# Performance work log

Measured on AMD Instinct MI355X. Metric: run time of the kernel, lower is better.

## Reference

```python
import jax, jax.numpy as jnp
import numpy as np
import math

INF = 10000000000.0
D_KEY = 64


def setup_inputs() -> dict:
    key = jax.random.key(0)
    kq, kk, kv = jax.random.split(key, 3)
    B, S, D = 4, 4096, D_KEY
    return {
        "query": jax.random.normal(kq, (B, S, D), dtype=jnp.float32),
        "key": jax.random.normal(kk, (B, S, D), dtype=jnp.float32),
        "value": jax.random.normal(kv, (B, S, D), dtype=jnp.float32),
    }


def reference(query, key, value):
    # dot_products: [B, Sq, Sk]
    scale = math.sqrt(D_KEY)
    scores = jnp.einsum("bqd,bkd->bqk", query, key)
    S = key.shape[1]
    # causal: subtract INF on strict upper triangle (triu(1)), before scaling
    tri = jnp.triu(jnp.full((S, S), INF, dtype=scores.dtype), k=1)
    scores = scores - tri[None, :, :]
    logits = scores / scale
    probs = jax.nn.softmax(logits, axis=-1)  # softmax over key dim
    # dropout p=0.0 -> identity
    return jnp.einsum("bqk,bkd->bqd", probs, value)
```

## Files before the change

kernel.cpp:

```cpp
#include <hip/hip_runtime.h>
#include <hip/hip_bf16.h>
#include <math.h>

#define B_  4
#define S_  4096
#define D_  64
#define NQT 64
#define NST 32
#define LDP 68
#define QSC 0.18033688f
#define M0  20.0f

typedef __attribute__((ext_vector_type(8))) short bf16x8;
typedef __attribute__((ext_vector_type(4))) float f32x4;
typedef __attribute__((ext_vector_type(4))) short short4v;

static __device__ inline short f2bf(float f) {
    union { float f; unsigned u; } v; v.f = f;
    unsigned u = v.u;
    unsigned r = u + 0x7fff + ((u >> 16) & 1);
    return (short)(r >> 16);
}
static __device__ inline float bf2f(short s) {
    union { unsigned u; float f; } v; v.u = ((unsigned)(unsigned short)s) << 16;
    return v.f;
}
static __device__ inline unsigned cvt_pk_bf16(float lo, float hi) {
    unsigned r;
    asm("v_cvt_pk_bf16_f32 %0, %1, %2" : "=v"(r) : "v"(lo), "v"(hi));
    return r;
}

__global__ __launch_bounds__(256) void fa_prep(const float* __restrict__ K,
                                               const float* __restrict__ V,
                                               short* __restrict__ Kbf,
                                               short* __restrict__ Vtbf)
{
    const int b   = blockIdx.x >> 6;
    const int st  = blockIdx.x & 63;
    const int tid = threadIdx.x;
    __shared__ short Vs[64 * 72];

    const size_t tbase = ((size_t)b * S_ + (size_t)st * 64) * D_;
    #pragma unroll
    for (int rr = 0; rr < 4; ++rr) {
        int i = tid + rr * 256;
        size_t e = tbase + (size_t)i * 4;
        f32x4 k = *(const f32x4*)(K + e);
        union { short4v s; unsigned u[2]; } ks;
        ks.u[0] = cvt_pk_bf16(k[0], k[1]);
        ks.u[1] = cvt_pk_bf16(k[2], k[3]);
        *(short4v*)(Kbf + e) = ks.s;
        f32x4 v = *(const f32x4*)(V + e);
        int key = i >> 4, d4 = (i & 15) * 4;
        Vs[(d4 + 0) * 72 + key] = f2bf(v[0]);
        Vs[(d4 + 1) * 72 + key] = f2bf(v[1]);
        Vs[(d4 + 2) * 72 + key] = f2bf(v[2]);
        Vs[(d4 + 3) * 72 + key] = f2bf(v[3]);
    }
    __syncthreads();
    #pragma unroll
    for (int cc = 0; cc < 2; ++cc) {
        int c = tid + cc * 256;
        int d = c >> 3, sg = c & 7;
        bf16x8 row = *(const bf16x8*)&Vs[d * 72 + sg * 8];
        *(bf16x8*)(Vtbf + ((size_t)(b * D_ + d)) * S_ + (size_t)st * 64 + sg * 8) = row;
    }
}

__global__ __launch_bounds__(512) void fa_part(const float* __restrict__ Qf,
                                               const short* __restrict__ Kbf,
                                               const short* __restrict__ Vtbf,
                                               short* __restrict__ Opart,
                                               float* __restrict__ Lpart,
                                               int CH, int T)
{
    const int bid = blockIdx.x;
    const int b   = bid / T;
    int r = bid - b * T;
    int qt2 = NST - 1;
    while (true) {
        int n = (2 * qt2 + 2 + CH - 1) / CH;
        if (r < n) break;
        r -= n; --qt2;
    }
    const int kt0 = r * CH;
    const int nkt = 2 * qt2 + 2;
    const int kt1 = (kt0 + CH < nkt) ? kt0 + CH : nkt;

    const int tid  = threadIdx.x;
    const int wave = tid >> 6;
    const int lane = tid & 63;
    const int lm   = lane & 15;
    const int lk   = lane >> 4;

    __shared__ __align__(16) short Ks[2][64 * 64];
    __shared__ __align__(16) short Vt[2][64 * 64];
    __shared__ __align__(16) short Ps[128 * LDP];

    bf16x8 qA[2];
    {
        const float* qp = Qf + ((size_t)(b * S_ + qt2 * 128 + wave * 16 + lm)) * D_;
        #pragma unroll
        for (int h = 0; h < 2; ++h) {
            f32x4 a0 = *(const f32x4*)(qp + h * 32 + lk * 8);
            f32x4 a1 = *(const f32x4*)(qp + h * 32 + lk * 8 + 4);
            union { bf16x8 v; unsigned u[4]; } qa;
            qa.u[0] = cvt_pk_bf16(a0[0] * QSC, a0[1] * QSC);
            qa.u[1] = cvt_pk_bf16(a0[2] * QSC, a0[3] * QSC);
            qa.u[2] = cvt_pk_bf16(a1[0] * QSC, a1[1] * QSC);
            qa.u[3] = cvt_pk_bf16(a1[2] * QSC, a1[3] * QSC);
            qA[h] = qa.v;
        }
    }

    bf16x8 onesF;
    #pragma unroll
    for (int j = 0; j < 8; ++j) onesF[j] = (short)0x3F80;

    const int srow = tid >> 3;
    const int sseg = (tid & 7) ^ (srow & 7);
    const char* kgp = (const char*)(Kbf + (size_t)b * S_ * D_)
                    + (size_t)(kt0 * 64 + srow) * 128 + sseg * 16;
    const char* vgp = (const char*)(Vtbf + ((size_t)(b * D_ + srow)) * S_)
                    + (size_t)kt0 * 128 + sseg * 16;

    bf16x8 kreg = *(const bf16x8*)kgp;
    bf16x8 vreg = *(const bf16x8*)vgp;
    kgp += 8192; vgp += 128;
    *(bf16x8*)&Ks[0][tid * 8] = kreg;
    *(bf16x8*)&Vt[0][tid * 8] = vreg;
    __syncthreads();
    if (kt0 + 1 < kt1) {
        kreg = *(const bf16x8*)kgp;
        vreg = *(const bf16x8*)vgp;
        kgp += 8192; vgp += 128;
    }

    f32x4 l4 = (f32x4){0.f, 0.f, 0.f, 0.f};
    f32x4 o_acc[4];
    #pragma unroll
    for (int dt = 0; dt < 4; ++dt) o_acc[dt] = (f32x4){0.f, 0.f, 0.f, 0.f};

    const int wrow = wave * 16 + lk * 4;
    int cur = 0;

    for (int kt = kt0; kt < kt1; ++kt) {
        f32x4 s4[4];
        __builtin_amdgcn_s_setprio(1);
        #pragma unroll
        for (int ct = 0; ct < 4; ++ct) {
            f32x4 acc = (f32x4){-M0, -M0, -M0, -M0};
            #pragma unroll
            for (int h = 0; h < 2; ++h) {
                int seg = (h * 4 + lk) ^ (lm & 7);
                bf16x8 bF = *(const bf16x8*)&Ks[cur][(ct * 16 + lm) * 64 + seg * 8];
                acc = __builtin_amdgcn_mfma_f32_16x16x32_bf16(qA[h], bF, acc, 0, 0, 0);
            }
            s4[ct] = acc;
        }
        __builtin_amdgcn_s_setprio(0);

        if (kt >= 2 * qt2) {
            const int koff = kt * 64 - qt2 * 128;
            #pragma unroll
            for (int ct = 0; ct < 4; ++ct) {
                #pragma unroll
                for (int rr = 0; rr < 4; ++rr) {
                    if (koff + ct * 16 + lm > wrow + rr) s4[ct][rr] = -INFINITY;
                }
            }
        }

        #pragma unroll
        for (int ct = 0; ct < 4; ++ct) {
            #pragma unroll
            for (int rr = 0; rr < 4; ++rr) s4[ct][rr] = exp2f(s4[ct][rr]);
        }
        #pragma unroll
        for (int ct = 0; ct < 4; ++ct) {
            unsigned p01 = cvt_pk_bf16(s4[ct][0], s4[ct][1]);
            unsigned p23 = cvt_pk_bf16(s4[ct][2], s4[ct][3]);
            Ps[(wrow + 0) * LDP + ct * 16 + lm] = (short)(p01 & 0xffff);
            Ps[(wrow + 1) * LDP + ct * 16 + lm] = (short)(p01 >> 16);
            Ps[(wrow + 2) * LDP + ct * 16 + lm] = (short)(p23 & 0xffff);
            Ps[(wrow + 3) * LDP + ct * 16 + lm] = (short)(p23 >> 16);
        }
        bf16x8 aF[2];
        #pragma unroll
        for (int kh = 0; kh < 2; ++kh)
            aF[kh] = *(const bf16x8*)&Ps[(wave * 16 + lm) * LDP + kh * 32 + lk * 8];
        __builtin_amdgcn_s_setprio(1);
        #pragma unroll
        for (int kh = 0; kh < 2; ++kh)
            l4 = __builtin_amdgcn_mfma_f32_16x16x32_bf16(aF[kh], onesF, l4, 0, 0, 0);
        #pragma unroll
        for (int dt = 0; dt < 4; ++dt) {
            #pragma unroll
            for (int kh = 0; kh < 2; ++kh) {
                int seg = (kh * 4 + lk) ^ (lm & 7);
                bf16x8 bF = *(const bf16x8*)&Vt[cur][(dt * 16 + lm) * 64 + seg * 8];
                o_acc[dt] = __builtin_amdgcn_mfma_f32_16x16x32_bf16(aF[kh], bF, o_acc[dt], 0, 0, 0);
            }
        }
        __builtin_amdgcn_s_setprio(0);

        if (kt + 1 < kt1) {
            *(bf16x8*)&Ks[cur ^ 1][tid * 8] = kreg;
            *(bf16x8*)&Vt[cur ^ 1][tid * 8] = vreg;
            __syncthreads();
            if (kt + 2 < kt1) {
                kreg = *(const bf16x8*)kgp;
                vreg = *(const bf16x8*)vgp;
                kgp += 8192; vgp += 128;
            }
            cur ^= 1;
        }
    }

    short* Op = Opart + (size_t)bid * (128 * D_);
    if (lm == 0) {
        #pragma unroll
        for (int rr = 0; rr < 4; ++rr)
            Lpart[(size_t)bid * 128 + wrow + rr] = l4[rr];
    }
    #pragma unroll
    for (int dt = 0; dt < 4; ++dt) {
        unsigned o01 = cvt_pk_bf16(o_acc[dt][0], o_acc[dt][1]);
        unsigned o23 = cvt_pk_bf16(o_acc[dt][2], o_acc[dt][3]);
        Op[(wrow + 0) * D_ + dt * 16 + lm] = (short)(o01 & 0xffff);
        Op[(wrow + 1) * D_ + dt * 16 + lm] = (short)(o01 >> 16);
        Op[(wrow + 2) * D_ + dt * 16 + lm] = (short)(o23 & 0xffff);
        Op[(wrow + 3) * D_ + dt * 16 + lm] = (short)(o23 >> 16);
    }
}

__global__ __launch_bounds__(256) void fa_combine(const short* __restrict__ Opart,
                                                  const float* __restrict__ Lpart,
                                                  float* __restrict__ O,
                                                  int CH, int T)
{
    const int idx = blockIdx.x * 256 + threadIdx.x;
    const int b   = idx / (S_ * 16);
    const int rem = idx - b * (S_ * 16);
    const int q   = rem >> 4;
    const int d4  = (rem & 15) << 2;
    const int qt2 = q >> 7;
    const int rit = q & 127;

    int F = 0;
    for (int y = qt2 + 1; y < NST; ++y) F += (2 * y + 2 + CH - 1) / CH;
    const int base = b * T + F;
    const int nch  = (2 * qt2 + 2 + CH - 1) / CH;

    float L = 0.f;
    f32x4 acc = (f32x4){0.f, 0.f, 0.f, 0.f};
    for (int c = 0; c < nch; ++c) {
        L += Lpart[(size_t)(base + c) * 128 + rit];
        short4v o = *(const short4v*)(Opart + (size_t)(base + c) * (128 * D_) + rit * D_ + d4);
        acc[0] += bf2f(o[0]); acc[1] += bf2f(o[1]);
        acc[2] += bf2f(o[2]); acc[3] += bf2f(o[3]);
    }
    float inv = 1.f / L;
    f32x4 outv;
    outv[0] = acc[0] * inv; outv[1] = acc[1] * inv;
    outv[2] = acc[2] * inv; outv[3] = acc[3] * inv;
    *(f32x4*)(O + (size_t)idx * 4) = outv;
}

__global__ __launch_bounds__(256) void fa_fwd(const float* __restrict__ Q,
                                              const float* __restrict__ K,
                                              const float* __restrict__ V,
                                              float* __restrict__ O)
{
    const int qt   = (gridDim.x - 1) - blockIdx.x;
    const int b    = blockIdx.y;
    const int tid  = threadIdx.x;
    const int wave = tid >> 6;
    const int lane = tid & 63;
    const int lm   = lane & 15;
    const int lk   = lane >> 4;

    __shared__ short Ks[64 * 72];
    __shared__ short Vt[64 * 72];
    __shared__ short Ps[64 * 72];

    const float* Qb = Q + ((size_t)b * S_ + (size_t)qt * 64) * D_;
    const float* Kb = K + (size_t)b * S_ * D_;
    const float* Vb = V + (size_t)b * S_ * D_;

    bf16x8 qA[2];
    {
        const float* qp = Qb + (wave * 16 + lm) * D_;
        #pragma unroll
        for (int h = 0; h < 2; ++h) {
            const float* p = qp + h * 32 + lk * 8;
            #pragma unroll
            for (int j = 0; j < 8; ++j) qA[h][j] = f2bf(p[j] * 0.125f);
        }
    }
    float m_i[4], l_i[4];
    f32x4 o_acc[4];
    #pragma unroll
    for (int rr = 0; rr < 4; ++rr) { m_i[rr] = -INFINITY; l_i[rr] = 0.f; }
    #pragma unroll
    for (int dt = 0; dt < 4; ++dt) o_acc[dt] = (f32x4){0.f, 0.f, 0.f, 0.f};

    const int n_kt = qt + 1;
    for (int kt = 0; kt < n_kt; ++kt) {
        __syncthreads();
        #pragma unroll
        for (int rr = 0; rr < 4; ++rr) {
            int i   = tid + rr * 256;
            int row = i >> 4;
            int c4  = (i & 15) * 4;
            const size_t gbase = ((size_t)(kt * 64 + row)) * D_ + c4;
            f32x4 kv = *(const f32x4*)(Kb + gbase);
            short4v ks;
            ks[0] = f2bf(kv[0]); ks[1] = f2bf(kv[1]);
            ks[2] = f2bf(kv[2]); ks[3] = f2bf(kv[3]);
            *(short4v*)&Ks[row * 72 + c4] = ks;
            f32x4 vv = *(const f32x4*)(Vb + gbase);
            Vt[(c4 + 0) * 72 + row] = f2bf(vv[0]);
            Vt[(c4 + 1) * 72 + row] = f2bf(vv[1]);
            Vt[(c4 + 2) * 72 + row] = f2bf(vv[2]);
            Vt[(c4 + 3) * 72 + row] = f2bf(vv[3]);
        }
        __syncthreads();
        f32x4 s4[4];
        #pragma unroll
        for (int ct = 0; ct < 4; ++ct) {
            f32x4 acc = (f32x4){0.f, 0.f, 0.f, 0.f};
            #pragma unroll
            for (int h = 0; h < 2; ++h) {
                bf16x8 bF = *(const bf16x8*)&Ks[(ct * 16 + lm) * 72 + h * 32 + lk * 8];
                acc = __builtin_amdgcn_mfma_f32_16x16x32_bf16(qA[h], bF, acc, 0, 0, 0);
            }
            s4[ct] = acc;
        }
        if (kt == qt) {
            #pragma unroll
            for (int ct = 0; ct < 4; ++ct) {
                #pragma unroll
                for (int rr = 0; rr < 4; ++rr) {
                    int qrow = wave * 16 + lk * 4 + rr;
                    int kcol = ct * 16 + lm;
                    if (kcol > qrow) s4[ct][rr] = -INFINITY;
                }
            }
        }
        float alpha[4];
        #pragma unroll
        for (int rr = 0; rr < 4; ++rr) {
            float mx = fmaxf(fmaxf(s4[0][rr], s4[1][rr]), fmaxf(s4[2][rr], s4[3][rr]));
            mx = fmaxf(mx, __shfl_xor(mx, 1));
            mx = fmaxf(mx, __shfl_xor(mx, 2));
            mx = fmaxf(mx, __shfl_xor(mx, 4));
            mx = fmaxf(mx, __shfl_xor(mx, 8));
            float mn = fmaxf(m_i[rr], mx);
            alpha[rr] = __expf(m_i[rr] - mn);
            m_i[rr] = mn;
        }
        float rsum[4] = {0.f, 0.f, 0.f, 0.f};
        #pragma unroll
        for (int ct = 0; ct < 4; ++ct) {
            #pragma unroll
            for (int rr = 0; rr < 4; ++rr) {
                float p = __expf(s4[ct][rr] - m_i[rr]);
                s4[ct][rr] = p;
                rsum[rr] += p;
            }
        }
        #pragma unroll
        for (int rr = 0; rr < 4; ++rr) {
            float rs = rsum[rr];
            rs += __shfl_xor(rs, 1);
            rs += __shfl_xor(rs, 2);
            rs += __shfl_xor(rs, 4);
            rs += __shfl_xor(rs, 8);
            l_i[rr] = l_i[rr] * alpha[rr] + rs;
        }
        #pragma unroll
        for (int ct = 0; ct < 4; ++ct) {
            #pragma unroll
            for (int rr = 0; rr < 4; ++rr) {
                Ps[(wave * 16 + lk * 4 + rr) * 72 + ct * 16 + lm] = f2bf(s4[ct][rr]);
            }
        }
        #pragma unroll
        for (int dt = 0; dt < 4; ++dt) {
            #pragma unroll
            for (int rr = 0; rr < 4; ++rr) o_acc[dt][rr] *= alpha[rr];
        }
        #pragma unroll
        for (int dt = 0; dt < 4; ++dt) {
            #pragma unroll
            for (int kh = 0; kh < 2; ++kh) {
                bf16x8 aF = *(const bf16x8*)&Ps[(wave * 16 + lm) * 72 + kh * 32 + lk * 8];
                bf16x8 bF = *(const bf16x8*)&Vt[(dt * 16 + lm) * 72 + kh * 32 + lk * 8];
                o_acc[dt] = __builtin_amdgcn_mfma_f32_16x16x32_bf16(aF, bF, o_acc[dt], 0, 0, 0);
            }
        }
    }
    float* Ob = O + ((size_t)b * S_ + (size_t)qt * 64) * D_;
    #pragma unroll
    for (int rr = 0; rr < 4; ++rr) {
        float inv = 1.f / l_i[rr];
        int row = wave * 16 + lk * 4 + rr;
        #pragma unroll
        for (int dt = 0; dt < 4; ++dt) {
            Ob[row * D_ + dt * 16 + lm] = o_acc[dt][rr] * inv;
        }
    }
}

extern "C" void kernel_launch(void* const* d_in, const int* in_sizes, int n_in,
                              void* d_out, int out_size, void* d_ws, size_t ws_size,
                              hipStream_t stream) {
    const float* Q = (const float*)d_in[0];
    const float* K = (const float*)d_in[1];
    const float* V = (const float*)d_in[2];
    float* O = (float*)d_out;

    const size_t convShorts = (size_t)B_ * S_ * D_;
    int CH = 0, T = 0;
    const int chs[5] = {6, 8, 16, 32, 64};
    for (int k = 0; k < 5; ++k) {
        int c = chs[k];
        int t = 0;
        for (int q2 = 0; q2 < NST; ++q2) t += (2 * q2 + 2 + c - 1) / c;
        size_t need = 2 * convShorts * 2
                    + (size_t)B_ * t * (128 * D_) * 2
                    + (size_t)B_ * t * 128 * 4;
        if (need <= ws_size) { CH = c; T = t; break; }
    }
    if (CH == 0) {
        dim3 grid(NQT, B_);
        fa_fwd<<<grid, 256, 0, stream>>>(Q, K, V, O);
        return;
    }
    short* Kbf   = (short*)d_ws;
    short* Vtbf  = Kbf + convShorts;
    short* Opart = Vtbf + convShorts;
    float* Lpart = (float*)(Opart + (size_t)B_ * T * (128 * D_));

    fa_prep<<<dim3(B_ * NQT), 256, 0, stream>>>(K, V, Kbf, Vtbf);
    fa_part<<<dim3(B_ * T), 512, 0, stream>>>(Q, Kbf, Vtbf, Opart, Lpart, CH, T);
    fa_combine<<<dim3((B_ * S_ * 16) / 256), 256, 0, stream>>>(Opart, Lpart, O, CH, T);
}
```

Before: 99.15 us.

## Compute transposed S tiles so P stays in registers, dropping the LDS round-trip

The QK^T MFMA now swaps its operands so each lane holds a row of the score tile laid out like the A operand of the PV MFMA. The probabilities are packed into bf16 fragments directly in registers instead of being written to and read back from shared memory. The V transpose in the prep kernel permutes key order within each tile to match this fragment layout, and the causal mask indexing is adjusted accordingly. It also removes the Ps LDS buffer and adds an occupancy hint to launch bounds, which may raise register pressure or cause spills.

```diff
diff --git a/kernel.cpp b/kernel.cpp
--- a/kernel.cpp
+++ b/kernel.cpp
@@ -7,7 +7,6 @@
 #define D_  64
 #define NQT 64
 #define NST 32
-#define LDP 68
 #define QSC 0.18033688f
 #define M0  20.0f
 
@@ -53,10 +52,11 @@
         *(short4v*)(Kbf + e) = ks.s;
         f32x4 v = *(const f32x4*)(V + e);
         int key = i >> 4, d4 = (i & 15) * 4;
-        Vs[(d4 + 0) * 72 + key] = f2bf(v[0]);
-        Vs[(d4 + 1) * 72 + key] = f2bf(v[1]);
-        Vs[(d4 + 2) * 72 + key] = f2bf(v[2]);
-        Vs[(d4 + 3) * 72 + key] = f2bf(v[3]);
+        int slot = (key & 32) + (((key & 15) >> 2) << 3) + (((key >> 4) & 1) << 2) + (key & 3);
+        Vs[(d4 + 0) * 72 + slot] = f2bf(v[0]);
+        Vs[(d4 + 1) * 72 + slot] = f2bf(v[1]);
+        Vs[(d4 + 2) * 72 + slot] = f2bf(v[2]);
+        Vs[(d4 + 3) * 72 + slot] = f2bf(v[3]);
     }
     __syncthreads();
     #pragma unroll
@@ -68,7 +68,7 @@
     }
 }
 
-__global__ __launch_bounds__(512) void fa_part(const float* __restrict__ Qf,
+__global__ __launch_bounds__(512, 6) void fa_part(const float* __restrict__ Qf,
                                                const short* __restrict__ Kbf,
                                                const short* __restrict__ Vtbf,
                                                short* __restrict__ Opart,
@@ -96,7 +96,6 @@
 
     __shared__ __align__(16) short Ks[2][64 * 64];
     __shared__ __align__(16) short Vt[2][64 * 64];
-    __shared__ __align__(16) short Ps[128 * LDP];
 
     bf16x8 qA[2];
     {
@@ -143,6 +142,7 @@
     for (int dt = 0; dt < 4; ++dt) o_acc[dt] = (f32x4){0.f, 0.f, 0.f, 0.f};
 
     const int wrow = wave * 16 + lk * 4;
+    const int qrow = wave * 16 + lm;
     int cur = 0;
 
     for (int kt = kt0; kt < kt1; ++kt) {
@@ -154,20 +154,20 @@
             #pragma unroll
             for (int h = 0; h < 2; ++h) {
                 int seg = (h * 4 + lk) ^ (lm & 7);
-                bf16x8 bF = *(const bf16x8*)&Ks[cur][(ct * 16 + lm) * 64 + seg * 8];
-                acc = __builtin_amdgcn_mfma_f32_16x16x32_bf16(qA[h], bF, acc, 0, 0, 0);
+                bf16x8 kF = *(const bf16x8*)&Ks[cur][(ct * 16 + lm) * 64 + seg * 8];
+                acc = __builtin_amdgcn_mfma_f32_16x16x32_bf16(kF, qA[h], acc, 0, 0, 0);
             }
             s4[ct] = acc;
         }
         __builtin_amdgcn_s_setprio(0);
 
         if (kt >= 2 * qt2) {
-            const int koff = kt * 64 - qt2 * 128;
+            const int koff = kt * 64 - qt2 * 128 + lk * 4;
             #pragma unroll
             for (int ct = 0; ct < 4; ++ct) {
                 #pragma unroll
                 for (int rr = 0; rr < 4; ++rr) {
-                    if (koff + ct * 16 + lm > wrow + rr) s4[ct][rr] = -INFINITY;
+                    if (koff + ct * 16 + rr > qrow) s4[ct][rr] = -INFINITY;
                 }
             }
         }
@@ -177,19 +177,16 @@
             #pragma unroll
             for (int rr = 0; rr < 4; ++rr) s4[ct][rr] = exp2f(s4[ct][rr]);
         }
-        #pragma unroll
-        for (int ct = 0; ct < 4; ++ct) {
-            unsigned p01 = cvt_pk_bf16(s4[ct][0], s4[ct][1]);
-            unsigned p23 = cvt_pk_bf16(s4[ct][2], s4[ct][3]);
-            Ps[(wrow + 0) * LDP + ct * 16 + lm] = (short)(p01 & 0xffff);
-            Ps[(wrow + 1) * LDP + ct * 16 + lm] = (short)(p01 >> 16);
-            Ps[(wrow + 2) * LDP + ct * 16 + lm] = (short)(p23 & 0xffff);
-            Ps[(wrow + 3) * LDP + ct * 16 + lm] = (short)(p23 >> 16);
-        }
         bf16x8 aF[2];
         #pragma unroll
-        for (int kh = 0; kh < 2; ++kh)
-            aF[kh] = *(const bf16x8*)&Ps[(wave * 16 + lm) * LDP + kh * 32 + lk * 8];
+        for (int kh = 0; kh < 2; ++kh) {
+            union { bf16x8 v; unsigned u[4]; } pa;
+            pa.u[0] = cvt_pk_bf16(s4[2 * kh][0],     s4[2 * kh][1]);
+            pa.u[1] = cvt_pk_bf16(s4[2 * kh][2],     s4[2 * kh][3]);
+            pa.u[2] = cvt_pk_bf16(s4[2 * kh + 1][0], s4[2 * kh + 1][1]);
+            pa.u[3] = cvt_pk_bf16(s4[2 * kh + 1][2], s4[2 * kh + 1][3]);
+            aF[kh] = pa.v;
+        }
         __builtin_amdgcn_s_setprio(1);
         #pragma unroll
         for (int kh = 0; kh < 2; ++kh)
```

Result: faster. 93.45 us, median of 2 (-5.8%).
